# Kernel optimization log

Hardware: AMD Instinct MI355X
Metric: run time of the kernel (lower is better)

## Reference

```python
import jax, jax.numpy as jnp
import numpy as np

V, E, H = 100000, 128, 256
P1, P2 = 512, 128
B, S, F = 256, 200, 10


def setup_inputs() -> dict:
    key = jax.random.key(0)
    ks = jax.random.split(key, 12)
    s = lambda *d: 1.0 / np.sqrt(d[-1])
    inp = {
        "x": jax.random.randint(ks[0], (B, S, F), 0, V),
        "emb": jax.random.normal(ks[1], (V, E), jnp.float32) * 0.1,
        # PyTorch LSTM params: gates ordered (i, f, g, o), shapes [4H, E] / [4H, H]
        "W_ih": jax.random.normal(ks[2], (4 * H, E), jnp.float32) * s(E),
        "W_hh": jax.random.normal(ks[3], (4 * H, H), jnp.float32) * s(H),
        "b_ih": jax.random.normal(ks[4], (4 * H,), jnp.float32) * s(H),
        "b_hh": jax.random.normal(ks[5], (4 * H,), jnp.float32) * s(H),
        "W1": jax.random.normal(ks[6], (H, P1), jnp.float32) * s(H),
        "b1": jnp.zeros((P1,), jnp.float32),
        "W2": jax.random.normal(ks[7], (P1, P2), jnp.float32) * s(P1),
        "b2": jnp.zeros((P2,), jnp.float32),
        "W3": jax.random.normal(ks[8], (P2, 1), jnp.float32) * s(P2),
        "b3": jnp.zeros((1,), jnp.float32),
    }
    return inp


def reference(x, emb, W_ih, W_hh, b_ih, b_hh, W1, b1, W2, b2, W3, b3):
    # embedding + mean over field dim -> [B, S, E]
    e = jnp.take(emb, x, axis=0).mean(axis=-2)
    T = e.shape[1] // 2
    hist, tgt = e[:, :T], e[:, T:2 * T]
    b = e.shape[0]
    h0 = jnp.zeros((b, H), e.dtype)
    c0 = jnp.zeros((b, H), e.dtype)

    def lstm_step(carry, xt):
        h, c = carry
        g = xt @ W_ih.T + h @ W_hh.T + b_ih + b_hh  # [B, 4H]
        gi, gf, gg, go = jnp.split(g, 4, axis=-1)
        c = jax.nn.sigmoid(gf) * c + jax.nn.sigmoid(gi) * jnp.tanh(gg)
        h = jax.nn.sigmoid(go) * jnpp_tanh(c) if False else jax.nn.sigmoid(go) * jnp.tanh(c)
        return (h, c), None

    (hN, cN), _ = jax.lax.scan(lstm_step, (h0, c0), jnp.swapaxes(hist, 0, 1))

    # Each target step restarts from the SAME history state (loop reuses history_state),
    # so all T target steps are independent single LSTM steps -> fully batched.
    g = jnp.einsum('bte,ge->btg', tgt, W_ih) + (hN @ W_hh.T)[:, None, :] + b_ih + b_hh
    gi, gf, gg, go = jnp.split(g, 4, axis=-1)
    c = jax.nn.sigmoid(gf) * cN[:, None, :] + jax.nn.sigmoid(gi) * jnp.tanh(gg)
    h = jax.nn.sigmoid(go) * jnp.tanh(c)  # [B, T, H]

    # PredictMLP (eval mode: dropout = identity), ReLU hidden activations
    z = jax.nn.relu(h @ W1 + b1)
    z = jax.nn.relu(z @ W2 + b2)
    out = jax.nn.sigmoid((z @ W3 + b3)[..., 0])  # [B, T]
    return out
```

## Files before the change

kernel.cpp:

```cpp
#include <hip/hip_runtime.h>
#include <hip/hip_bf16.h>
#include <math.h>

#define B_  256
#define S_  200
#define F_  10
#define T_  100
#define E_  128
#define H_  256
#define G4  1024
#define P1_ 512
#define P2_ 128

typedef __attribute__((ext_vector_type(8))) short short8;
typedef __attribute__((ext_vector_type(4))) float f32x4;
typedef _Float16 half2f __attribute__((ext_vector_type(2)));

#if __has_builtin(__builtin_amdgcn_fdot2)
#define FDOT2(w2, h2, acc) __builtin_amdgcn_fdot2((w2), (h2), (acc), false)
#else
#define FDOT2(w2, h2, acc) ((acc) + (float)((w2)[0]) * (float)((h2)[0]) + (float)((w2)[1]) * (float)((h2)[1]))
#endif
#define BCH2(u) __builtin_bit_cast(half2f, (u))

#define NL2_ 36
#define NV2_ 92

__device__ __forceinline__ float fsig(float x) { return 1.0f / (1.0f + __expf(-x)); }
__device__ __forceinline__ float ftanh(float x) { return 1.0f - 2.0f / (__expf(2.0f * x) + 1.0f); }
__device__ __forceinline__ float bf2f(ushort u) { return __uint_as_float(((uint)u) << 16); }
__device__ __forceinline__ ushort f2bf(float f) {
    __hip_bfloat16 v = __float2bfloat16(f);
    return *(ushort*)&v;
}
__device__ __forceinline__ ushort f2h(float f) {
    _Float16 h = (_Float16)f;
    return __builtin_bit_cast(ushort, h);
}
__device__ __forceinline__ float h2f(ushort u) {
    return (float)__builtin_bit_cast(_Float16, u);
}

__global__ __launch_bounds__(256) void k_prep_all(
    const float* __restrict__ W_hh, uint* __restrict__ WPu,
    const float* __restrict__ W1, ushort* __restrict__ W1T,
    const float* __restrict__ W2, ushort* __restrict__ W2T,
    const float* __restrict__ W_ih, ushort* __restrict__ Wihb,
    ushort* __restrict__ Whhb,
    const float* __restrict__ b_ih, const float* __restrict__ b_hh,
    float* __restrict__ bsum,
    const int* __restrict__ x, const float* __restrict__ emb,
    ushort* __restrict__ ebf)
{
    __shared__ float t[32][33];
    int blk = blockIdx.x;
    int tid = threadIdx.x;
    if (blk < 256) {
        int k0 = (blk & 7) * 32, c0 = (blk >> 3) * 32;
        int lk = tid & 31, lc8 = tid >> 5;
        #pragma unroll
        for (int i = 0; i < 4; ++i)
            t[lc8 + 8 * i][lk] = W_hh[(long)(c0 + lc8 + 8 * i) * 256 + k0 + lk];
        __syncthreads();
        int kpl = tid >> 4, ccl = tid & 15;
        #pragma unroll
        for (int hf = 0; hf < 2; ++hf) {
            int c = ccl + 16 * hf;
            uint lo = f2h(t[c][2 * kpl]);
            uint hi = f2h(t[c][2 * kpl + 1]);
            WPu[(long)(k0 / 2 + kpl) * G4 + c0 + c] = lo | (hi << 16);
        }
    } else if (blk < 448) {
        const float* W; ushort* WT; int R, C, idx;
        if (blk < 384) { W = W1; WT = W1T; R = H_;  C = P1_; idx = blk - 256;
                         idx = (idx & 15) | ((idx >> 4) << 8); }
        else           { W = W2; WT = W2T; R = P1_; C = P2_; idx = blk - 384;
                         idx = (idx & 3) | ((idx >> 2) << 8); }
        int c0 = (idx & 255) * 32, r0 = (idx >> 8) * 32;
        int lc = tid & 31, lr = tid >> 5;
        #pragma unroll
        for (int i = 0; i < 4; ++i)
            t[lr + 8 * i][lc] = W[(long)(r0 + lr + 8 * i) * C + c0 + lc];
        __syncthreads();
        #pragma unroll
        for (int i = 0; i < 4; ++i)
            WT[(long)(c0 + lr + 8 * i) * R + r0 + lc] = f2bf(t[lc][lr + 8 * i]);
    } else if (blk < 960) {
        int i = (blk - 448) * 256 + tid;
        Wihb[i] = f2bf(W_ih[i]);
    } else if (blk < 1984) {
        int i = (blk - 960) * 256 + tid;
        Whhb[i] = f2bf(W_hh[i]);
    } else if (blk < 1988) {
        int i = (blk - 1984) * 256 + tid;
        bsum[i] = b_ih[i] + b_hh[i];
    } else {
        int bs = (blk - 1988) * 2 + (tid >> 7);
        int e  = tid & 127;
        const int* xr = x + (long)bs * F_;
        float acc = 0.f;
        #pragma unroll
        for (int f = 0; f < F_; ++f) acc += emb[(long)xr[f] * E_ + e];
        ebf[(long)bs * E_ + e] = f2bf(acc * (1.0f / F_));
    }
}

template<int ACT, int OUTM>
__global__ __launch_bounds__(256) void k_gemm_mfma(
    const ushort* __restrict__ A, int rowDiv, long sOuter, long sInner,
    const ushort* __restrict__ Bm,
    const float* __restrict__ bias,
    const float* __restrict__ rowAdd, int rowAddDiv,
    void* __restrict__ Cout, int N, int K)
{
    constexpr int LDT = 40;
    __shared__ ushort Al[128 * LDT];
    __shared__ ushort Bl[128 * LDT];
    int tid = threadIdx.x;
    int n0 = blockIdx.x * 128;
    int m0 = blockIdx.y * 128;

    int rA = tid >> 2, qA = tid & 3;
    int m_lo = m0 + rA, m_hi = m_lo + 64;
    long a0 = (long)(m_lo / rowDiv) * sOuter + (long)(m_lo % rowDiv) * sInner + qA * 8;
    long a1 = (long)(m_hi / rowDiv) * sOuter + (long)(m_hi % rowDiv) * sInner + qA * 8;
    const ushort* b0p = Bm + (long)(n0 + rA) * K + qA * 8;
    const ushort* b1p = Bm + (long)(n0 + rA + 64) * K + qA * 8;

    int lane = tid & 63, wave = tid >> 6;
    int wr = wave >> 1, wc = wave & 1;
    int lrow = lane & 15, lkh = lane >> 4;

    const f32x4 fz = {0.f, 0.f, 0.f, 0.f};
    f32x4 acc[4][4];
    #pragma unroll
    for (int i = 0; i < 4; ++i)
        #pragma unroll
        for (int j = 0; j < 4; ++j) acc[i][j] = fz;

    int nk = K >> 5;
    for (int kc = 0; kc < nk; ++kc) {
        uint4 va0 = *(const uint4*)(A + a0 + kc * 32);
        uint4 va1 = *(const uint4*)(A + a1 + kc * 32);
        uint4 vb0 = *(const uint4*)(b0p + kc * 32);
        uint4 vb1 = *(const uint4*)(b1p + kc * 32);
        *(uint4*)&Al[rA * LDT + qA * 8]        = va0;
        *(uint4*)&Al[(rA + 64) * LDT + qA * 8] = va1;
        *(uint4*)&Bl[rA * LDT + qA * 8]        = vb0;
        *(uint4*)&Bl[(rA + 64) * LDT + qA * 8] = vb1;
        __syncthreads();
        short8 af[4], bfr[4];
        #pragma unroll
        for (int mi = 0; mi < 4; ++mi)
            af[mi] = *(const short8*)&Al[(wr * 64 + mi * 16 + lrow) * LDT + lkh * 8];
        #pragma unroll
        for (int ni = 0; ni < 4; ++ni)
            bfr[ni] = *(const short8*)&Bl[(wc * 64 + ni * 16 + lrow) * LDT + lkh * 8];
        #pragma unroll
        for (int mi = 0; mi < 4; ++mi)
            #pragma unroll
            for (int ni = 0; ni < 4; ++ni)
                acc[mi][ni] = __builtin_amdgcn_mfma_f32_16x16x32_bf16(
                    af[mi], bfr[ni], acc[mi][ni], 0, 0, 0);
        __syncthreads();
    }
    #pragma unroll
    for (int mi = 0; mi < 4; ++mi) {
        #pragma unroll
        for (int r = 0; r < 4; ++r) {
            int m = m0 + wr * 64 + mi * 16 + lkh * 4 + r;
            long rowoff = rowAdd ? (long)(m / rowAddDiv) * N : 0;
            #pragma unroll
            for (int ni = 0; ni < 4; ++ni) {
                int n = n0 + wc * 64 + ni * 16 + lrow;
                float v = acc[mi][ni][r];
                if (bias)   v += bias[n];
                if (rowAdd) v += rowAdd[rowoff + n];
                if (ACT)    v = fmaxf(v, 0.f);
                if (OUTM == 1)      ((ushort*)Cout)[(long)m * N + n] = f2bf(v);
                else if (OUTM == 2) ((ushort*)Cout)[(long)m * N + n] = f2h(v);
                else                ((float*)Cout)[(long)m * N + n] = v;
            }
        }
    }
}

__global__ __launch_bounds__(256) void k_gdec_fused(
    const ushort* __restrict__ A, int rowDiv, long sOuter, long sInner,
    const ushort* __restrict__ Bm,
    const float* __restrict__ hhdec,
    const float* __restrict__ cNb,
    ushort* __restrict__ hdec)
{
    constexpr int LDT = 40;
    __shared__ ushort Al[128 * LDT];
    __shared__ ushort Bl[128 * LDT];
    __shared__ ushort Zl[128 * 132];
    int tid = threadIdx.x;
    int j0 = blockIdx.x * 32;
    int m0 = blockIdx.y * 128;
    const int K = E_;

    int rA = tid >> 2, qA = tid & 3;
    int m_lo = m0 + rA, m_hi = m_lo + 64;
    long a0 = (long)(m_lo / rowDiv) * sOuter + (long)(m_lo % rowDiv) * sInner + qA * 8;
    long a1 = (long)(m_hi / rowDiv) * sOuter + (long)(m_hi % rowDiv) * sInner + qA * 8;
    int nr0 = rA, nr1 = rA + 64;
    const ushort* b0p = Bm + (long)((nr0 >> 5) * 256 + j0 + (nr0 & 31)) * K + qA * 8;
    const ushort* b1p = Bm + (long)((nr1 >> 5) * 256 + j0 + (nr1 & 31)) * K + qA * 8;

    int lane = tid & 63, wave = tid >> 6;
    int wr = wave >> 1, wc = wave & 1;
    int lrow = lane & 15, lkh = lane >> 4;

    const f32x4 fz = {0.f, 0.f, 0.f, 0.f};
    f32x4 acc[4][4];
    #pragma unroll
    for (int i = 0; i < 4; ++i)
        #pragma unroll
        for (int j = 0; j < 4; ++j) acc[i][j] = fz;

    for (int kc = 0; kc < K / 32; ++kc) {
        uint4 va0 = *(const uint4*)(A + a0 + kc * 32);
        uint4 va1 = *(const uint4*)(A + a1 + kc * 32);
        uint4 vb0 = *(const uint4*)(b0p + kc * 32);
        uint4 vb1 = *(const uint4*)(b1p + kc * 32);
        *(uint4*)&Al[rA * LDT + qA * 8]        = va0;
        *(uint4*)&Al[(rA + 64) * LDT + qA * 8] = va1;
        *(uint4*)&Bl[rA * LDT + qA * 8]        = vb0;
        *(uint4*)&Bl[(rA + 64) * LDT + qA * 8] = vb1;
        __syncthreads();
        short8 af[4], bfr[4];
        #pragma unroll
        for (int mi = 0; mi < 4; ++mi)
            af[mi] = *(const short8*)&Al[(wr * 64 + mi * 16 + lrow) * LDT + lkh * 8];
        #pragma unroll
        for (int ni = 0; ni < 4; ++ni)
            bfr[ni] = *(const short8*)&Bl[(wc * 64 + ni * 16 + lrow) * LDT + lkh * 8];
        #pragma unroll
        for (int mi = 0; mi < 4; ++mi)
            #pragma unroll
            for (int ni = 0; ni < 4; ++ni)
                acc[mi][ni] = __builtin_amdgcn_mfma_f32_16x16x32_bf16(
                    af[mi], bfr[ni], acc[mi][ni], 0, 0, 0);
        __syncthreads();
    }
    #pragma unroll
    for (int mi = 0; mi < 4; ++mi) {
        #pragma unroll
        for (int r = 0; r < 4; ++r) {
            int row = wr * 64 + mi * 16 + lkh * 4 + r;
            int bidx = (m0 + row) / T_;
            #pragma unroll
            for (int ni = 0; ni < 4; ++ni) {
                int col = wc * 64 + ni * 16 + lrow;
                float v = acc[mi][ni][r]
                        + hhdec[(long)bidx * G4 + (col >> 5) * 256 + j0 + (col & 31)];
                Zl[row * 132 + col] = f2bf(v);
            }
        }
    }
    __syncthreads();
    int jl = tid & 31, mb = tid >> 5;
    #pragma unroll
    for (int q = 0; q < 16; ++q) {
        int row = mb * 16 + q;
        int m = m0 + row;
        int bidx = m / T_;
        float gi = bf2f(Zl[row * 132 +      jl]);
        float gf = bf2f(Zl[row * 132 + 32 + jl]);
        float gg = bf2f(Zl[row * 132 + 64 + jl]);
        float go = bf2f(Zl[row * 132 + 96 + jl]);
        float cv = fsig(gf) * cNb[(long)bidx * H_ + j0 + jl] + fsig(gi) * ftanh(gg);
        hdec[(long)m * H_ + j0 + jl] = f2bf(fsig(go) * ftanh(cv));
    }
}

__global__ __launch_bounds__(256) void k_z2_fused(
    const ushort* __restrict__ A, const ushort* __restrict__ Bm,
    const float* __restrict__ b2, const float* __restrict__ W3,
    const float* __restrict__ b3, float* __restrict__ out)
{
    constexpr int LDT = 40;
    __shared__ ushort Al[128 * LDT];
    __shared__ ushort Bl[128 * LDT];
    __shared__ float Zl[128 * 132];
    int tid = threadIdx.x;
    int m0 = blockIdx.x * 128;
    const int K = P1_;

    int rA = tid >> 2, qA = tid & 3;
    const ushort* a0p = A + (long)(m0 + rA) * K + qA * 8;
    const ushort* a1p = A + (long)(m0 + rA + 64) * K + qA * 8;
    const ushort* b0p = Bm + (long)rA * K + qA * 8;
    const ushort* b1p = Bm + (long)(rA + 64) * K + qA * 8;

    int lane = tid & 63, wave = tid >> 6;
    int wr = wave >> 1, wc = wave & 1;
    int lrow = lane & 15, lkh = lane >> 4;

    const f32x4 fz = {0.f, 0.f, 0.f, 0.f};
    f32x4 acc[4][4];
    #pragma unroll
    for (int i = 0; i < 4; ++i)
        #pragma unroll
        for (int j = 0; j < 4; ++j) acc[i][j] = fz;

    for (int kc = 0; kc < K / 32; ++kc) {
        uint4 va0 = *(const uint4*)(a0p + kc * 32);
        uint4 va1 = *(const uint4*)(a1p + kc * 32);
        uint4 vb0 = *(const uint4*)(b0p + kc * 32);
        uint4 vb1 = *(const uint4*)(b1p + kc * 32);
        *(uint4*)&Al[rA * LDT + qA * 8]        = va0;
        *(uint4*)&Al[(rA + 64) * LDT + qA * 8] = va1;
        *(uint4*)&Bl[rA * LDT + qA * 8]        = vb0;
        *(uint4*)&Bl[(rA + 64) * LDT + qA * 8] = vb1;
        __syncthreads();
        short8 af[4], bfr[4];
        #pragma unroll
        for (int mi = 0; mi < 4; ++mi)
            af[mi] = *(const short8*)&Al[(wr * 64 + mi * 16 + lrow) * LDT + lkh * 8];
        #pragma unroll
        for (int ni = 0; ni < 4; ++ni)
            bfr[ni] = *(const short8*)&Bl[(wc * 64 + ni * 16 + lrow) * LDT + lkh * 8];
        #pragma unroll
        for (int mi = 0; mi < 4; ++mi)
            #pragma unroll
            for (int ni = 0; ni < 4; ++ni)
                acc[mi][ni] = __builtin_amdgcn_mfma_f32_16x16x32_bf16(
                    af[mi], bfr[ni], acc[mi][ni], 0, 0, 0);
        __syncthreads();
    }
    #pragma unroll
    for (int mi = 0; mi < 4; ++mi) {
        #pragma unroll
        for (int r = 0; r < 4; ++r) {
            int row = wr * 64 + mi * 16 + lkh * 4 + r;
            #pragma unroll
            for (int ni = 0; ni < 4; ++ni) {
                int col = wc * 64 + ni * 16 + lrow;
                Zl[row * 132 + col] = fmaxf(acc[mi][ni][r] + b2[col], 0.f);
            }
        }
    }
    __syncthreads();
    float w3a = W3[lane], w3b = W3[64 + lane], b3v = b3[0];
    for (int r = 0; r < 32; ++r) {
        int row = wave * 32 + r;
        float s = Zl[row * 132 + lane] * w3a + Zl[row * 132 + 64 + lane] * w3b;
        #pragma unroll
        for (int off = 32; off > 0; off >>= 1) s += __shfl_down(s, off);
        if (lane == 0) out[m0 + row] = fsig(s + b3v);
    }
}

__global__ __launch_bounds__(512, 2) void k_lstm_scan(
    const ushort* __restrict__ Xgh, const uint* __restrict__ WPu,
    float* __restrict__ hN, float* __restrict__ cN, ushort* __restrict__ hNb)
{
    extern __shared__ __align__(16) char smem[];
    uint*   Wl    = (uint*)smem;
    float*  act_s = (float*)(smem + NL2_ * 4096);
    uint*   h16u  = (uint*)(act_s + G4);
    ushort* h16   = (ushort*)h16u;
    int tid = threadIdx.x;
    int b   = blockIdx.x;
    int cB  = tid + 512;

    for (int i = tid; i < NL2_ * 1024; i += 512) {
        int row = i >> 10, col = i & 1023;
        Wl[col * NL2_ + row] = WPu[(long)row * G4 + col];
    }
    uint wrA[NV2_], wrB[NV2_];
    #pragma unroll
    for (int i = 0; i < NV2_; ++i) {
        wrA[i] = WPu[(long)(NL2_ + i) * G4 + tid];
        wrB[i] = WPu[(long)(NL2_ + i) * G4 + cB];
    }
    if (tid < 128) h16u[tid] = 0;
    float c_r = 0.f;
    __syncthreads();

    int isTanhB = (tid >> 8) == 0;
    const ushort* xgp = Xgh + (long)b * T_ * G4;
    const uint* wcA = Wl + tid * NL2_;
    const uint* wcB = Wl + (tid + 512) * NL2_;

    for (int t = 0; t < T_; ++t) {
        float xvA = h2f(xgp[(long)t * G4 + tid]);
        float xvB = h2f(xgp[(long)t * G4 + cB]);
        float aA0 = 0.f, aA1 = 0.f, aB0 = 0.f, aB1 = 0.f;
        #pragma unroll
        for (int r4 = 0; r4 < NL2_ / 4; ++r4) {
            uint4 hh = *(const uint4*)(h16u + 4 * r4);
            uint4 wa = *(const uint4*)(wcA + 4 * r4);
            uint4 wb = *(const uint4*)(wcB + 4 * r4);
            aA0 = FDOT2(BCH2(wa.x), BCH2(hh.x), aA0); aB0 = FDOT2(BCH2(wb.x), BCH2(hh.x), aB0);
            aA1 = FDOT2(BCH2(wa.y), BCH2(hh.y), aA1); aB1 = FDOT2(BCH2(wb.y), BCH2(hh.y), aB1);
            aA0 = FDOT2(BCH2(wa.z), BCH2(hh.z), aA0); aB0 = FDOT2(BCH2(wb.z), BCH2(hh.z), aB0);
            aA1 = FDOT2(BCH2(wa.w), BCH2(hh.w), aA1); aB1 = FDOT2(BCH2(wb.w), BCH2(hh.w), aB1);
        }
        #pragma unroll
        for (int r4 = 0; r4 < NV2_ / 4; ++r4) {
            uint4 hh = *(const uint4*)(h16u + NL2_ + 4 * r4);
            aA0 = FDOT2(BCH2(wrA[4 * r4 + 0]), BCH2(hh.x), aA0);
            aB0 = FDOT2(BCH2(wrB[4 * r4 + 0]), BCH2(hh.x), aB0);
            aA1 = FDOT2(BCH2(wrA[4 * r4 + 1]), BCH2(hh.y), aA1);
            aB1 = FDOT2(BCH2(wrB[4 * r4 + 1]), BCH2(hh.y), aB1);
            aA0 = FDOT2(BCH2(wrA[4 * r4 + 2]), BCH2(hh.z), aA0);
            aB0 = FDOT2(BCH2(wrB[4 * r4 + 2]), BCH2(hh.z), aB0);
            aA1 = FDOT2(BCH2(wrA[4 * r4 + 3]), BCH2(hh.w), aA1);
            aB1 = FDOT2(BCH2(wrB[4 * r4 + 3]), BCH2(hh.w), aB1);
        }
        float aA = aA0 + aA1, aB = aB0 + aB1;
        act_s[tid] = fsig(aA + xvA);
        float gB = aB + xvB;
        act_s[cB] = isTanhB ? ftanh(gB) : fsig(gB);
        __syncthreads();
        if (tid < H_) {
            float cn = act_s[H_ + tid] * c_r + act_s[tid] * act_s[2 * H_ + tid];
            c_r = cn;
            float h = act_s[3 * H_ + tid] * ftanh(cn);
            h16[tid] = f2h(h);
            if (t == T_ - 1) {
                hN[(long)b * H_ + tid] = h;
                cN[(long)b * H_ + tid] = c_r;
                hNb[(long)b * H_ + tid] = f2bf(h);
            }
        }
        __syncthreads();
    }
}

extern "C" void kernel_launch(void* const* d_in, const int* in_sizes, int n_in,
                              void* d_out, int out_size, void* d_ws, size_t ws_size,
                              hipStream_t stream)
{
    const int*   x    = (const int*)d_in[0];
    const float* emb  = (const float*)d_in[1];
    const float* W_ih = (const float*)d_in[2];
    const float* W_hh = (const float*)d_in[3];
    const float* b_ih = (const float*)d_in[4];
    const float* b_hh = (const float*)d_in[5];
    const float* W1   = (const float*)d_in[6];
    const float* b1   = (const float*)d_in[7];
    const float* W2   = (const float*)d_in[8];
    const float* b2   = (const float*)d_in[9];
    const float* W3   = (const float*)d_in[10];
    const float* b3   = (const float*)d_in[11];
    float* out = (float*)d_out;

    float* ws = (float*)d_ws;
    ushort* ebf   = (ushort*)ws;
    ushort* Xgh   = (ushort*)(ws + 3276800);
    ushort* hdecb = (ushort*)(ws + 16384000);
    ushort* z1b   = (ushort*)(ws + 19660800);
    float* bsum  = ws + 26214400;
    float* hN    = bsum + 1024;
    float* cN    = hN + 65536;
    ushort* hNb  = (ushort*)(cN + 65536);
    float* hhdec = cN + 65536 + 32768;
    uint*  WPu   = (uint*)(hhdec + 262144);
    ushort* Wihb = (ushort*)(WPu + 131072);
    ushort* Whhb = Wihb + 131072;
    ushort* W1T  = Whhb + 262144;
    ushort* W2T  = W1T + 131072;

    k_prep_all<<<1988 + B_ * S_ / 2, 256, 0, stream>>>(
        W_hh, WPu, W1, W1T, W2, W2T, W_ih, Wihb, Whhb,
        b_ih, b_hh, bsum, x, emb, ebf);

    k_gemm_mfma<0, 2><<<dim3(G4 / 128, (B_ * T_) / 128), 256, 0, stream>>>(
        ebf, T_, (long)S_ * E_, (long)E_, Wihb, bsum, nullptr, 1,
        Xgh, G4, E_);

    size_t scan_smem = (size_t)NL2_ * 4096 + G4 * sizeof(float) + 128 * sizeof(uint);
    k_lstm_scan<<<B_, 512, scan_smem, stream>>>(Xgh, WPu, hN, cN, hNb);

    k_gemm_mfma<0, 0><<<dim3(G4 / 128, B_ / 128), 256, 0, stream>>>(
        hNb, B_, 0L, (long)H_, Whhb, bsum, nullptr, 1,
        hhdec, G4, H_);

    k_gdec_fused<<<dim3(H_ / 32, (B_ * T_) / 128), 256, 0, stream>>>(
        ebf + T_ * E_, T_, (long)S_ * E_, (long)E_, Wihb, hhdec, cN, hdecb);

    k_gemm_mfma<1, 1><<<dim3(P1_ / 128, (B_ * T_) / 128), 256, 0, stream>>>(
        hdecb, B_ * T_, 0L, (long)H_, W1T, b1, nullptr, 1,
        z1b, P1_, H_);

    k_z2_fused<<<(B_ * T_) / 128, 256, 0, stream>>>(z1b, W2T, b2, W3, b3, out);
}
```

Baseline: 378.5 us.

## Fuse MLP layer-1 GEMM into layer-2/3 kernel keeping z1 in LDS

Replaces the separate W1 GEMM plus the z2 kernel with one kernel per 128-row tile that computes relu(h@W1+b1) into shared memory as bf16, then runs the W2 GEMM reading A straight from LDS, then the W3 dot and sigmoid. This removes the global write and read of the 25600x512 z1 intermediate and one launch. The LSTM scan also stops writing the unused fp32 hN. The trade-off is a large LDS footprint (about 153KB) limiting each CU to one block, and only 200 blocks doing four sequential N-tiles each, with no overlap of loads and MFMA.

```diff
diff --git a/kernel.cpp b/kernel.cpp
--- a/kernel.cpp
+++ b/kernel.cpp
@@ -276,53 +276,93 @@
     }
 }
 
-__global__ __launch_bounds__(256) void k_z2_fused(
-    const ushort* __restrict__ A, const ushort* __restrict__ Bm,
-    const float* __restrict__ b2, const float* __restrict__ W3,
-    const float* __restrict__ b3, float* __restrict__ out)
+#define Z1S 520
+__global__ __launch_bounds__(256) void k_mlp_fused(
+    const ushort* __restrict__ A,
+    const ushort* __restrict__ W1T,
+    const float* __restrict__ b1,
+    const ushort* __restrict__ W2T,
+    const float* __restrict__ b2,
+    const float* __restrict__ W3, const float* __restrict__ b3,
+    float* __restrict__ out)
 {
-    constexpr int LDT = 40;
-    __shared__ ushort Al[128 * LDT];
-    __shared__ ushort Bl[128 * LDT];
-    __shared__ float Zl[128 * 132];
+    extern __shared__ __align__(16) char smem[];
+    ushort* z1l = (ushort*)smem;
+    ushort* Al  = z1l + 128 * Z1S;
+    ushort* Bl  = Al + 128 * 40;
     int tid = threadIdx.x;
     int m0 = blockIdx.x * 128;
-    const int K = P1_;
 
     int rA = tid >> 2, qA = tid & 3;
-    const ushort* a0p = A + (long)(m0 + rA) * K + qA * 8;
-    const ushort* a1p = A + (long)(m0 + rA + 64) * K + qA * 8;
-    const ushort* b0p = Bm + (long)rA * K + qA * 8;
-    const ushort* b1p = Bm + (long)(rA + 64) * K + qA * 8;
-
     int lane = tid & 63, wave = tid >> 6;
     int wr = wave >> 1, wc = wave & 1;
     int lrow = lane & 15, lkh = lane >> 4;
-
     const f32x4 fz = {0.f, 0.f, 0.f, 0.f};
+
+    for (int nt = 0; nt < 4; ++nt) {
+        f32x4 acc[4][4];
+        #pragma unroll
+        for (int i = 0; i < 4; ++i)
+            #pragma unroll
+            for (int j = 0; j < 4; ++j) acc[i][j] = fz;
+        for (int kc = 0; kc < H_ / 32; ++kc) {
+            uint4 va0 = *(const uint4*)(A + (long)(m0 + rA) * H_ + kc * 32 + qA * 8);
+            uint4 va1 = *(const uint4*)(A + (long)(m0 + rA + 64) * H_ + kc * 32 + qA * 8);
+            uint4 vb0 = *(const uint4*)(W1T + (long)(nt * 128 + rA) * H_ + kc * 32 + qA * 8);
+            uint4 vb1 = *(const uint4*)(W1T + (long)(nt * 128 + rA + 64) * H_ + kc * 32 + qA * 8);
+            *(uint4*)&Al[rA * 40 + qA * 8]        = va0;
+            *(uint4*)&Al[(rA + 64) * 40 + qA * 8] = va1;
+            *(uint4*)&Bl[rA * 40 + qA * 8]        = vb0;
+            *(uint4*)&Bl[(rA + 64) * 40 + qA * 8] = vb1;
+            __syncthreads();
+            short8 af[4], bfr[4];
+            #pragma unroll
+            for (int mi = 0; mi < 4; ++mi)
+                af[mi] = *(const short8*)&Al[(wr * 64 + mi * 16 + lrow) * 40 + lkh * 8];
+            #pragma unroll
+            for (int ni = 0; ni < 4; ++ni)
+                bfr[ni] = *(const short8*)&Bl[(wc * 64 + ni * 16 + lrow) * 40 + lkh * 8];
+            #pragma unroll
+            for (int mi = 0; mi < 4; ++mi)
+                #pragma unroll
+                for (int ni = 0; ni < 4; ++ni)
+                    acc[mi][ni] = __builtin_amdgcn_mfma_f32_16x16x32_bf16(
+                        af[mi], bfr[ni], acc[mi][ni], 0, 0, 0);
+            __syncthreads();
+        }
+        #pragma unroll
+        for (int mi = 0; mi < 4; ++mi) {
+            #pragma unroll
+            for (int r = 0; r < 4; ++r) {
+                int row = wr * 64 + mi * 16 + lkh * 4 + r;
+                #pragma unroll
+                for (int ni = 0; ni < 4; ++ni) {
+                    int col = nt * 128 + wc * 64 + ni * 16 + lrow;
+                    z1l[row * Z1S + col] = f2bf(fmaxf(acc[mi][ni][r] + b1[col], 0.f));
+                }
+            }
+        }
+    }
+    __syncthreads();
+
     f32x4 acc[4][4];
     #pragma unroll
     for (int i = 0; i < 4; ++i)
         #pragma unroll
         for (int j = 0; j < 4; ++j) acc[i][j] = fz;
-
-    for (int kc = 0; kc < K / 32; ++kc) {
-        uint4 va0 = *(const uint4*)(a0p + kc * 32);
-        uint4 va1 = *(const uint4*)(a1p + kc * 32);
-        uint4 vb0 = *(const uint4*)(b0p + kc * 32);
-        uint4 vb1 = *(const uint4*)(b1p + kc * 32);
-        *(uint4*)&Al[rA * LDT + qA * 8]        = va0;
-        *(uint4*)&Al[(rA + 64) * LDT + qA * 8] = va1;
-        *(uint4*)&Bl[rA * LDT + qA * 8]        = vb0;
-        *(uint4*)&Bl[(rA + 64) * LDT + qA * 8] = vb1;
+    for (int kc = 0; kc < P1_ / 32; ++kc) {
+        uint4 vb0 = *(const uint4*)(W2T + (long)rA * P1_ + kc * 32 + qA * 8);
+        uint4 vb1 = *(const uint4*)(W2T + (long)(rA + 64) * P1_ + kc * 32 + qA * 8);
+        *(uint4*)&Bl[rA * 40 + qA * 8]        = vb0;
+        *(uint4*)&Bl[(rA + 64) * 40 + qA * 8] = vb1;
         __syncthreads();
         short8 af[4], bfr[4];
         #pragma unroll
         for (int mi = 0; mi < 4; ++mi)
-            af[mi] = *(const short8*)&Al[(wr * 64 + mi * 16 + lrow) * LDT + lkh * 8];
+            af[mi] = *(const short8*)&z1l[(wr * 64 + mi * 16 + lrow) * Z1S + kc * 32 + lkh * 8];
         #pragma unroll
         for (int ni = 0; ni < 4; ++ni)
-            bfr[ni] = *(const short8*)&Bl[(wc * 64 + ni * 16 + lrow) * LDT + lkh * 8];
+            bfr[ni] = *(const short8*)&Bl[(wc * 64 + ni * 16 + lrow) * 40 + lkh * 8];
         #pragma unroll
         for (int mi = 0; mi < 4; ++mi)
             #pragma unroll
@@ -331,6 +371,7 @@
                     af[mi], bfr[ni], acc[mi][ni], 0, 0, 0);
         __syncthreads();
     }
+    float* Zf = (float*)z1l;
     #pragma unroll
     for (int mi = 0; mi < 4; ++mi) {
         #pragma unroll
@@ -339,7 +380,7 @@
             #pragma unroll
             for (int ni = 0; ni < 4; ++ni) {
                 int col = wc * 64 + ni * 16 + lrow;
-                Zl[row * 132 + col] = fmaxf(acc[mi][ni][r] + b2[col], 0.f);
+                Zf[row * 132 + col] = fmaxf(acc[mi][ni][r] + b2[col], 0.f);
             }
         }
     }
@@ -347,7 +388,7 @@
     float w3a = W3[lane], w3b = W3[64 + lane], b3v = b3[0];
     for (int r = 0; r < 32; ++r) {
         int row = wave * 32 + r;
-        float s = Zl[row * 132 + lane] * w3a + Zl[row * 132 + 64 + lane] * w3b;
+        float s = Zf[row * 132 + lane] * w3a + Zf[row * 132 + 64 + lane] * w3b;
         #pragma unroll
         for (int off = 32; off > 0; off >>= 1) s += __shfl_down(s, off);
         if (lane == 0) out[m0 + row] = fsig(s + b3v);
@@ -356,7 +397,7 @@
 
 __global__ __launch_bounds__(512, 2) void k_lstm_scan(
     const ushort* __restrict__ Xgh, const uint* __restrict__ WPu,
-    float* __restrict__ hN, float* __restrict__ cN, ushort* __restrict__ hNb)
+    float* __restrict__ cN, ushort* __restrict__ hNb)
 {
     extern __shared__ __align__(16) char smem[];
     uint*   Wl    = (uint*)smem;
@@ -423,7 +464,6 @@
             float h = act_s[3 * H_ + tid] * ftanh(cn);
             h16[tid] = f2h(h);
             if (t == T_ - 1) {
-                hN[(long)b * H_ + tid] = h;
                 cN[(long)b * H_ + tid] = c_r;
                 hNb[(long)b * H_ + tid] = f2bf(h);
             }
@@ -454,10 +494,8 @@
     ushort* ebf   = (ushort*)ws;
     ushort* Xgh   = (ushort*)(ws + 3276800);
     ushort* hdecb = (ushort*)(ws + 16384000);
-    ushort* z1b   = (ushort*)(ws + 19660800);
     float* bsum  = ws + 26214400;
-    float* hN    = bsum + 1024;
-    float* cN    = hN + 65536;
+    float* cN    = bsum + 1024;
     ushort* hNb  = (ushort*)(cN + 65536);
     float* hhdec = cN + 65536 + 32768;
     uint*  WPu   = (uint*)(hhdec + 262144);
@@ -475,7 +513,7 @@
         Xgh, G4, E_);
 
     size_t scan_smem = (size_t)NL2_ * 4096 + G4 * sizeof(float) + 128 * sizeof(uint);
-    k_lstm_scan<<<B_, 512, scan_smem, stream>>>(Xgh, WPu, hN, cN, hNb);
+    k_lstm_scan<<<B_, 512, scan_smem, stream>>>(Xgh, WPu, cN, hNb);
 
     k_gemm_mfma<0, 0><<<dim3(G4 / 128, B_ / 128), 256, 0, stream>>>(
         hNb, B_, 0L, (long)H_, Whhb, bsum, nullptr, 1,
@@ -484,9 +522,7 @@
     k_gdec_fused<<<dim3(H_ / 32, (B_ * T_) / 128), 256, 0, stream>>>(
         ebf + T_ * E_, T_, (long)S_ * E_, (long)E_, Wihb, hhdec, cN, hdecb);
 
-    k_gemm_mfma<1, 1><<<dim3(P1_ / 128, (B_ * T_) / 128), 256, 0, stream>>>(
-        hdecb, B_ * T_, 0L, (long)H_, W1T, b1, nullptr, 1,
-        z1b, P1_, H_);
-
-    k_z2_fused<<<(B_ * T_) / 128, 256, 0, stream>>>(z1b, W2T, b2, W3, b3, out);
-}
+    size_t mlp_smem = (size_t)128 * Z1S * 2 + 2 * 128 * 40 * 2;
+    k_mlp_fused<<<(B_ * T_) / 128, 256, mlp_smem, stream>>>(
+        hdecb, W1T, b1, W2T, b2, W3, b3, out);
+}
```

Result: faster. 357.6 us, median of 2 (-5.5%).
